# Performance work log

Hardware: AMD Instinct MI355X
Metric: run time of the kernel (lower is better)

The kernel has to match this reference:

```python
import jax, jax.numpy as jnp
import numpy as np

GROUP_NORM_EPSILON = 1e-06
NUM_GROUPS = 32


def group_norm(x, gamma, beta, num_groups, eps):
    # x: [B, H, W, C]; normalize over (H, W, C//G) within each group.
    B, H, W, C = x.shape
    xg = x.reshape(B, H, W, num_groups, C // num_groups)
    mean = jnp.mean(xg, axis=(1, 2, 4), keepdims=True)
    var = jnp.mean(jnp.square(xg - mean), axis=(1, 2, 4), keepdims=True)
    xn = (xg - mean) * jax.lax.rsqrt(var + eps)
    return xn.reshape(B, H, W, C) * gamma + beta


def setup_inputs() -> dict:
    key = jax.random.key(0)
    ks = jax.random.split(key, 6)
    B, H, W, C = 4, 64, 64, 512
    scale = 1.0 / np.sqrt(C)
    return {
        "inputs": jax.random.normal(ks[0], (B, H, W, C), dtype=jnp.float32),
        "gamma": jnp.ones((C,), dtype=jnp.float32),
        "beta": jnp.zeros((C,), dtype=jnp.float32),
        "Wq": jax.random.normal(ks[1], (C, C), dtype=jnp.float32) * scale,
        "bq": jnp.zeros((C,), dtype=jnp.float32),
        "Wk": jax.random.normal(ks[2], (C, C), dtype=jnp.float32) * scale,
        "bk": jnp.zeros((C,), dtype=jnp.float32),
        "Wv": jax.random.normal(ks[3], (C, C), dtype=jnp.float32) * scale,
        "bv": jnp.zeros((C,), dtype=jnp.float32),
        "Wo": jax.random.normal(ks[4], (C, C), dtype=jnp.float32) * scale,
        "bo": jnp.zeros((C,), dtype=jnp.float32),
    }


def reference(inputs, gamma, beta, Wq, bq, Wk, bk, Wv, bv, Wo, bo):
    B, H, W, C = inputs.shape
    N = H * W
    h = group_norm(inputs, gamma, beta, NUM_GROUPS, GROUP_NORM_EPSILON)
    hf = h.reshape(B, N, C)  # flatten spatial: [B, N, C]
    q = hf @ Wq + bq
    k = hf @ Wk + bk
    v = hf @ Wv + bv
    # full spatial self-attention: [B, N, N]
    scores = jnp.einsum("bnc,bmc->bnm", q, k) * (C ** -0.5)
    attn = jax.nn.softmax(scores, axis=-1)
    out = jnp.einsum("bnm,bmc->bnc", attn, v)
    out = out @ Wo + bo
    return out.reshape(B, H, W, C) + inputs
```

## Files before the change

### kernel.cpp

```cpp
#include <hip/hip_runtime.h>
#include <hip/hip_bf16.h>

using bf16 = __hip_bfloat16;
using u16  = unsigned short;
typedef __attribute__((ext_vector_type(8))) short s16x8;
typedef __attribute__((ext_vector_type(4))) float f32x4;

__device__ __forceinline__ float b2f(u16 u){
  union{unsigned u; float f;} c; c.u = ((unsigned)u)<<16; return c.f;
}
__device__ __forceinline__ u16 f2b(float f){
  __hip_bfloat16 h = __float2bfloat16(f);
  return *reinterpret_cast<u16*>(&h);
}

#define GLDS16(g, l_) __builtin_amdgcn_global_load_lds( \
    (const __attribute__((address_space(1))) unsigned int*)(g), \
    (__attribute__((address_space(3))) unsigned int*)(l_), 16, 0, 0)

__global__ __launch_bounds__(512) void gn_kernel(const float* __restrict__ x,
    const float* __restrict__ gamma, const float* __restrict__ beta,
    bf16* __restrict__ h)
{
  const int b = blockIdx.x >> 5, g = blockIdx.x & 31;
  const int t = threadIdx.x;
  const size_t base = (size_t)b*4096*512 + (size_t)g*16;
  float sum = 0.f, sq = 0.f;
  for (int i = 0; i < 8; i++){
    const float* p = x + base + (size_t)(i*512 + t)*512;
    #pragma unroll
    for (int j = 0; j < 4; j++){
      f32x4 v = *(const f32x4*)(p + j*4);
      #pragma unroll
      for (int e = 0; e < 4; e++){ sum += v[e]; sq += v[e]*v[e]; }
    }
  }
  __shared__ float red[16];
  for (int o = 32; o > 0; o >>= 1){ sum += __shfl_xor(sum, o); sq += __shfl_xor(sq, o); }
  const int w = t >> 6, l = t & 63;
  if (l == 0){ red[w] = sum; red[8 + w] = sq; }
  __syncthreads();
  if (t == 0){
    float a = 0.f, bb = 0.f;
    for (int i = 0; i < 8; i++){ a += red[i]; bb += red[8 + i]; }
    red[0] = a; red[8] = bb;
  }
  __syncthreads();
  const float inv_n = 1.f/65536.f;
  const float mean = red[0]*inv_n;
  const float var  = red[8]*inv_n - mean*mean;
  const float rstd = rsqrtf(var + 1e-6f);
  float ga[16], be[16];
  #pragma unroll
  for (int j = 0; j < 16; j++){
    ga[j] = gamma[g*16 + j];
    be[j] = beta [g*16 + j];
  }
  u16* hp = (u16*)h;
  for (int i = 0; i < 8; i++){
    const float* p = x + base + (size_t)(i*512 + t)*512;
    u16* q = hp + base + (size_t)(i*512 + t)*512;
    s16x8 o0, o1;
    #pragma unroll
    for (int j = 0; j < 4; j++){
      f32x4 v = *(const f32x4*)(p + j*4);
      #pragma unroll
      for (int e = 0; e < 4; e++){
        int c = j*4 + e;
        u16 r = f2b((v[e] - mean)*rstd*ga[c] + be[c]);
        if (c < 8) o0[c] = (short)r; else o1[c - 8] = (short)r;
      }
    }
    *(s16x8*)q = o0; *(s16x8*)(q + 8) = o1;
  }
}

struct W4 { const float* p[4]; };
__global__ __launch_bounds__(256) void transpose_w4(W4 srcs, bf16* __restrict__ dst)
{
  __shared__ float tile[64][65];
  const float* in = srcs.p[blockIdx.z];
  u16* out = (u16*)dst + (size_t)blockIdx.z*512*512;
  const int tr = blockIdx.y*64, tc = blockIdx.x*64;
  const int t = threadIdx.x;
  #pragma unroll
  for (int i = 0; i < 16; i++){
    int idx = i*256 + t, r = idx >> 6, c = idx & 63;
    tile[r][c] = in[(size_t)(tr + r)*512 + tc + c];
  }
  __syncthreads();
  #pragma unroll
  for (int i = 0; i < 16; i++){
    int idx = i*256 + t, r = idx >> 6, c = idx & 63;
    out[(size_t)(tc + r)*512 + tr + c] = f2b(tile[c][r]);
  }
}

template<int EPI, typename OutT>
__global__ __launch_bounds__(256) void gemm_bt(
    const u16* __restrict__ A, int lda, long sA,
    const u16* __restrict__ Bt, int ldb, long sB,
    OutT* __restrict__ Cmat, int ldc, long sC,
    int K, float scale,
    const float* __restrict__ b0, const float* __restrict__ res)
{
  __shared__ u16 As[128*64];
  __shared__ u16 Bs[128*64];
  const int t = threadIdx.x, l = t & 63, w = t >> 6;
  const int wr = w >> 1, wc = w & 1;
  int bx = blockIdx.x, by = blockIdx.y;
  {
    const int gx = gridDim.x, nb = gx * gridDim.y;
    if ((nb & 7) == 0){
      int lin = by*gx + bx;
      int s = (lin & 7)*(nb >> 3) + (lin >> 3);
      bx = s % gx; by = s / gx;
    }
  }
  const int m0 = by * 128, n0 = bx * 128;
  const u16* Au  = A  + (size_t)blockIdx.z * sA;
  const u16* Btu = Bt + (size_t)blockIdx.z * sB;

  f32x4 acc[4][4];
  #pragma unroll
  for (int m = 0; m < 4; m++)
    #pragma unroll
    for (int n = 0; n < 4; n++) acc[m][n] = (f32x4){0.f,0.f,0.f,0.f};

  const int srow = l >> 3;
  const int scol = ((l & 7) ^ srow) * 8;
  const int xorv = (l & 7) << 4;
  const int nkt = K >> 6;
  for (int kt = 0; kt < nkt; ++kt){
    const int k0 = kt << 6;
    #pragma unroll
    for (int j = 0; j < 4; j++){
      const int chunk = w*4 + j;
      const int row = chunk*8 + srow;
      GLDS16(Au  + (size_t)(m0 + row)*lda + k0 + scol, &As[chunk*512]);
      GLDS16(Btu + (size_t)(n0 + row)*ldb + k0 + scol, &Bs[chunk*512]);
    }
    __syncthreads();
    #pragma unroll
    for (int kk = 0; kk < 2; kk++){
      const int kbyte = (kk*64 + (l >> 4)*16) ^ xorv;
      s16x8 af[4], bff[4];
      #pragma unroll
      for (int m = 0; m < 4; m++)
        af[m]  = *(const s16x8*)((const char*)As + (wr*64 + m*16 + (l & 15))*128 + kbyte);
      #pragma unroll
      for (int n = 0; n < 4; n++)
        bff[n] = *(const s16x8*)((const char*)Bs + (wc*64 + n*16 + (l & 15))*128 + kbyte);
      #pragma unroll
      for (int m = 0; m < 4; m++)
        #pragma unroll
        for (int n = 0; n < 4; n++)
          acc[m][n] = __builtin_amdgcn_mfma_f32_16x16x32_bf16(af[m], bff[n], acc[m][n], 0, 0, 0);
    }
    __syncthreads();
  }
  const int lc = l & 15, lr4 = (l >> 4)*4;
  OutT* Cz = Cmat + (size_t)blockIdx.z * sC;
  #pragma unroll
  for (int n = 0; n < 4; n++){
    const int col = n0 + wc*64 + n*16 + lc;
    const float bv = (EPI & 1) ? b0[col] : 0.f;
    #pragma unroll
    for (int m = 0; m < 4; m++){
      const int rowb = m0 + wr*64 + m*16 + lr4;
      #pragma unroll
      for (int r = 0; r < 4; r++){
        float v = acc[m][n][r];
        if (EPI & 2) v *= scale;
        v += bv;
        const size_t off = (size_t)(rowb + r)*ldc + col;
        if (EPI & 4) v += res[off];
        if constexpr (__is_same(OutT, float)) Cz[off] = v;
        else ((u16*)Cz)[off] = f2b(v);
      }
    }
  }
}

template<int EPI, int OMODE>
__global__ __launch_bounds__(512, 2) void gemm256(
    const u16* __restrict__ A, int lda, long sA,
    const u16* __restrict__ Bt, int ldb, long sB,
    u16* __restrict__ C0, int ldc, long sC,
    u16* __restrict__ C1, u16* __restrict__ C2,
    int K, float scale,
    const float* __restrict__ b0, const float* __restrict__ b1,
    const float* __restrict__ b2)
{
  __shared__ u16 L[2][2][2][256*32];
  const int t = threadIdx.x, l = t & 63, w = t >> 6;
  const int wm = w >> 2, wn = w & 3;
  int bx = blockIdx.x, by = blockIdx.y;
  {
    const int gx = gridDim.x, nb = gx * gridDim.y;
    if ((nb & 7) == 0){
      int lin = by*gx + bx;
      int s = (lin & 7)*(nb >> 3) + (lin >> 3);
      bx = s % gx; by = s / gx;
    }
  }
  const int m0 = by * 256, n0 = bx * 256;
  const u16* Au  = A  + (size_t)blockIdx.z * sA;
  const u16* Btu = Bt + (size_t)blockIdx.z * sB;

  f32x4 acc[8][4];
  #pragma unroll
  for (int m = 0; m < 8; m++)
    #pragma unroll
    for (int n = 0; n < 4; n++) acc[m][n] = (f32x4){0.f,0.f,0.f,0.f};

  const int srow_s = t >> 2;
  const int sce    = (((t & 3)*16) ^ (((srow_s >> 1) & 3) << 4)) >> 1;
  const int l15 = l & 15, kb16 = (l >> 4)*16;

  int arow[8], brow[4];
  #pragma unroll
  for (int i = 0; i < 8; i++){
    const int r = wm*128 + i*16 + l15;
    arow[i] = r*64 + (kb16 ^ (((r >> 1) & 3) << 4));
  }
  #pragma unroll
  for (int i = 0; i < 4; i++){
    const int r = wn*64 + i*16 + l15;
    brow[i] = r*64 + (kb16 ^ (((r >> 1) & 3) << 4));
  }

#define STG256(HALF, XU, LD, ROW0, COLBASE) do { \
    GLDS16((XU) + (size_t)((ROW0) + srow_s)*(LD) + (COLBASE) + sce, \
           (char*)(HALF) + w*1024); \
    GLDS16((XU) + (size_t)((ROW0) + 128 + srow_s)*(LD) + (COLBASE) + sce, \
           (char*)(HALF) + 8192 + w*1024); \
  } while(0)

#define VMW4 asm volatile("s_waitcnt vmcnt(4)" ::: "memory")

#define PH256(BUF, KK, MQ, STAGE_STMT, WAIT_STMT) do { \
    s16x8 af_[4], bg_[4]; \
    _Pragma("unroll") \
    for (int mf = 0; mf < 4; mf++) \
      af_[mf] = *(const s16x8*)((const char*)&L[BUF][0][KK][0] + arow[(MQ)*4 + mf]); \
    _Pragma("unroll") \
    for (int nf = 0; nf < 4; nf++) \
      bg_[nf] = *(const s16x8*)((const char*)&L[BUF][1][KK][0] + brow[nf]); \
    STAGE_STMT; \
    WAIT_STMT; \
    __builtin_amdgcn_s_barrier(); \
    __builtin_amdgcn_s_setprio(1); \
    _Pragma("unroll") \
    for (int mf = 0; mf < 4; mf++) \
      _Pragma("unroll") \
      for (int nf = 0; nf < 4; nf++) \
        acc[(MQ)*4 + mf][nf] = __builtin_amdgcn_mfma_f32_16x16x32_bf16( \
            af_[mf], bg_[nf], acc[(MQ)*4 + mf][nf], 0, 0, 0); \
    __builtin_amdgcn_s_setprio(0); \
    __builtin_amdgcn_s_barrier(); \
  } while(0)

  const int nkt = K >> 6;
  STG256(&L[0][0][0][0], Au,  lda, m0, 0);
  STG256(&L[0][1][0][0], Btu, ldb, n0, 0);
  STG256(&L[0][0][1][0], Au,  lda, m0, 32);
  STG256(&L[0][1][1][0], Btu, ldb, n0, 32);
  STG256(&L[1][0][0][0], Au,  lda, m0, 64);
  STG256(&L[1][1][0][0], Btu, ldb, n0, 64);
  VMW4;
  __builtin_amdgcn_s_barrier();

  const int niter = nkt >> 1;
  for (int it = 0; it < niter; ++it){
    const int kt1 = 2*it + 1;
    const int kA  = (kt1 + 1 < nkt) ? kt1 + 1 : nkt - 1;
    const int kB  = (kt1 + 2 < nkt) ? kt1 + 2 : nkt - 1;
    PH256(0, 0, 0, STG256(&L[1][0][1][0], Au,  lda, m0, kt1*64 + 32), (void)0);
    PH256(0, 0, 1, STG256(&L[1][1][1][0], Btu, ldb, n0, kt1*64 + 32), (void)0);
    PH256(0, 1, 0, STG256(&L[0][0][0][0], Au,  lda, m0, kA*64),       (void)0);
    PH256(0, 1, 1, STG256(&L[0][1][0][0], Btu, ldb, n0, kA*64),       VMW4);
    PH256(1, 0, 0, STG256(&L[0][0][1][0], Au,  lda, m0, kA*64 + 32),  (void)0);
    PH256(1, 0, 1, STG256(&L[0][1][1][0], Btu, ldb, n0, kA*64 + 32),  (void)0);
    PH256(1, 1, 0, STG256(&L[1][0][0][0], Au,  lda, m0, kB*64),       (void)0);
    PH256(1, 1, 1, STG256(&L[1][1][0][0], Btu, ldb, n0, kB*64),       VMW4);
  }

  asm volatile("s_waitcnt vmcnt(0)" ::: "memory");
  __builtin_amdgcn_s_barrier();
  u16* Lb = (u16*)&L[0][0][0][0];
  const int lr4 = (l >> 4)*4;
  #pragma unroll
  for (int nf = 0; nf < 4; nf++){
    const int cloc = wn*64 + nf*16 + l15;
    const int colg = n0 + cloc;
    float bv = 0.f;
    if (EPI & 8){
      const float* bp = (colg < 512) ? b0 : (colg < 1024 ? b1 : b2);
      bv = bp[colg & 511];
    } else if (EPI & 1) bv = b0[colg];
    #pragma unroll
    for (int mf = 0; mf < 8; mf++){
      const int rl0 = wm*128 + mf*16 + lr4;
      #pragma unroll
      for (int r = 0; r < 4; r++){
        float v = acc[mf][nf][r];
        if (EPI & 2) v *= scale;
        v += bv;
        const int row = rl0 + r;
        const int byte = row*512 + ((cloc*2) ^ (((row >> 3) & 7) << 4));
        *(u16*)((char*)Lb + byte) = f2b(v);
      }
    }
  }
  __syncthreads();
  if (OMODE == 0){
    u16* Cz = C0 + (size_t)blockIdx.z * sC;
    #pragma unroll
    for (int i = 0; i < 16; i++){
      const int idx = i*512 + t;
      const int row = idx >> 5, cb = (idx & 31)*16;
      const int byte = row*512 + (cb ^ (((row >> 3) & 7) << 4));
      s16x8 v = *(const s16x8*)((const char*)Lb + byte);
      *(s16x8*)(Cz + (size_t)(m0 + row)*ldc + n0 + (cb >> 1)) = v;
    }
  } else {
    const int sec = n0 >> 9, wc0 = n0 & 511;
    if (sec < 2){
      u16* dst = (sec == 0) ? C0 : C1;
      #pragma unroll
      for (int i = 0; i < 16; i++){
        const int idx = i*512 + t;
        const int row = idx >> 5, cb = (idx & 31)*16;
        const int byte = row*512 + (cb ^ (((row >> 3) & 7) << 4));
        s16x8 v = *(const s16x8*)((const char*)Lb + byte);
        *(s16x8*)(dst + (size_t)(m0 + row)*512 + wc0 + (cb >> 1)) = v;
      }
    } else {
      const int batch = m0 >> 12, ntok = m0 & 4095;
      u16* dst = C2 + (size_t)batch*512*4096;
      #pragma unroll
      for (int i = 0; i < 16; i++){
        const int idx = i*512 + t;
        const int c_loc = idx >> 5, rseg = (idx & 31)*8;
        s16x8 v;
        #pragma unroll
        for (int j = 0; j < 8; j++){
          const int row = rseg + j;
          const int byte = row*512 + ((c_loc*2) ^ (((row >> 3) & 7) << 4));
          v[j] = *(const short*)((const char*)Lb + byte);
        }
        *(s16x8*)(dst + (size_t)(wc0 + c_loc)*4096 + ntok + rseg) = v;
      }
    }
  }
#undef STG256
#undef VMW4
#undef PH256
}

__global__ __launch_bounds__(512) void pv_fused(
    const u16* __restrict__ S, const u16* __restrict__ vT,
    bf16* __restrict__ ao, int batched, int batch0)
{
  __shared__ u16 Bs[256*64];
  __shared__ u16 Ps[64*64];
  __shared__ float lsArr[64];
  const int t = threadIdx.x, l = t & 63, w = t >> 6;
  int batch, mt, half;
  if (batched){
    const int lin = blockIdx.x, x = lin & 7, s = lin >> 3;
    batch = x >> 1; mt = (s >> 1)*2 + (x & 1); half = s & 1;
  } else { batch = batch0; mt = blockIdx.x >> 1; half = blockIdx.x & 1; }
  const int m0 = mt*64, c0 = half*256;
  const u16* Sb  = S  + (size_t)batch*4096*4096;
  const u16* vTb = vT + (size_t)batch*512*4096 + (size_t)c0*4096;
  u16* aob = (u16*)ao + (size_t)batch*4096*512;

  f32x4 acc[4][2];
  #pragma unroll
  for (int m = 0; m < 4; m++)
    #pragma unroll
    for (int n = 0; n < 2; n++) acc[m][n] = (f32x4){0.f,0.f,0.f,0.f};

  const int srow = l >> 3, lane8 = l & 7;
  const int scol = (lane8 ^ srow) * 8;
  const int xorv = lane8 << 4;
  const int r_loc = w*8 + srow;
  const int smaddr = r_loc*128 + ((lane8*16) ^ (srow << 4));
  float lsumrow = 0.f;

  const u16* Srow = Sb + (size_t)(m0 + r_loc)*4096 + lane8*8;

  #pragma unroll
  for (int j = 0; j < 4; j++){
    const int chunk = w*4 + j;
    const int row = chunk*8 + srow;
    GLDS16(vTb + (size_t)row*4096 + scol, &Bs[chunk*512]);
  }
  s16x8 S_cur = *(const s16x8*)Srow;

  for (int kt = 0; kt < 64; ++kt){
    const int ktn = (kt < 63) ? kt + 1 : 63;
    s16x8 S_next = *(const s16x8*)(Srow + ktn*64);

    s16x8 pb;
    #pragma unroll
    for (int j = 0; j < 8; j++){
      const float pvv = exp2f(fminf(b2f((u16)S_cur[j]), 100.f));
      lsumrow += pvv;
      pb[j] = (short)f2b(pvv);
    }

    *(s16x8*)((char*)Ps + smaddr) = pb;

    asm volatile("s_waitcnt lgkmcnt(0)" ::: "memory");
    __builtin_amdgcn_sched_barrier(0);
    asm volatile("s_waitcnt vmcnt(1)" ::: "memory");
    __builtin_amdgcn_sched_barrier(0);
    __builtin_amdgcn_s_barrier();

    #pragma unroll
    for (int kk = 0; kk < 2; kk++){
      const int kbyte = (kk*64 + (l >> 4)*16) ^ xorv;
      s16x8 pa[4], bf2[2];
      #pragma unroll
      for (int m = 0; m < 4; m++)
        pa[m] = *(const s16x8*)((const char*)Ps + (m*16 + (l & 15))*128 + kbyte);
      #pragma unroll
      for (int n = 0; n < 2; n++)
        bf2[n] = *(const s16x8*)((const char*)Bs + (w*32 + n*16 + (l & 15))*128 + kbyte);
      #pragma unroll
      for (int m = 0; m < 4; m++)
        #pragma unroll
        for (int n = 0; n < 2; n++)
          acc[m][n] = __builtin_amdgcn_mfma_f32_16x16x32_bf16(pa[m], bf2[n], acc[m][n], 0, 0, 0);
    }

    __builtin_amdgcn_sched_barrier(0);
    __builtin_amdgcn_s_barrier();
    __builtin_amdgcn_sched_barrier(0);

    #pragma unroll
    for (int j = 0; j < 4; j++){
      const int chunk = w*4 + j;
      const int row = chunk*8 + srow;
      GLDS16(vTb + (size_t)row*4096 + ktn*64 + scol, &Bs[chunk*512]);
    }
    S_cur = S_next;
  }

  lsumrow += __shfl_xor(lsumrow, 1);
  lsumrow += __shfl_xor(lsumrow, 2);
  lsumrow += __shfl_xor(lsumrow, 4);
  if (lane8 == 0) lsArr[r_loc] = lsumrow;
  __syncthreads();
  #pragma unroll
  for (int m = 0; m < 4; m++){
    const f32x4 lq = *(const f32x4*)&lsArr[m*16 + (l >> 4)*4];
    #pragma unroll
    for (int r = 0; r < 4; r++){
      const float inv = 1.f / lq[r];
      const int row = m0 + m*16 + (l >> 4)*4 + r;
      #pragma unroll
      for (int n = 0; n < 2; n++){
        const int col = c0 + w*32 + n*16 + (l & 15);
        aob[(size_t)row*512 + col] = f2b(acc[m][n][r] * inv);
      }
    }
  }
}

extern "C" void kernel_launch(void* const* d_in, const int* in_sizes, int n_in,
                              void* d_out, int out_size, void* d_ws, size_t ws_size,
                              hipStream_t stream)
{
  (void)in_sizes; (void)n_in; (void)out_size;
  const float* x     = (const float*)d_in[0];
  const float* gamma = (const float*)d_in[1];
  const float* beta  = (const float*)d_in[2];
  const float* Wq = (const float*)d_in[3]; const float* bq = (const float*)d_in[4];
  const float* Wk = (const float*)d_in[5]; const float* bk = (const float*)d_in[6];
  const float* Wv = (const float*)d_in[7]; const float* bv = (const float*)d_in[8];
  const float* Wo = (const float*)d_in[9]; const float* bo = (const float*)d_in[10];
  float* out = (float*)d_out;

  const int B = 4, N = 4096, C = 512;
  const long NC = (long)N*C;
  const float scl2 = 0.04419417382415922f * 1.4426950408889634f;

  char* p0 = (char*)d_ws;
  auto align = [](size_t b){ return (b + 255) & ~(size_t)255; };
  const size_t sz_h  = align((size_t)B*NC*2);
  const size_t sz_w  = align((size_t)4*C*C*2);
  const size_t sz_q  = align((size_t)B*NC*2);
  const size_t sz_S  = align((size_t)B*N*N*2);
  const size_t need_full = sz_h + sz_w + 4*sz_q + sz_S;

  bf16* h    = (bf16*)p0;
  bf16* wAll = (bf16*)(p0 + sz_h);
  char* pv   = p0 + sz_h + sz_w;
  bf16* woT  = wAll + (size_t)3*C*C;

  gn_kernel<<<dim3(B*32), dim3(512), 0, stream>>>(x, gamma, beta, h);
  W4 ws4; ws4.p[0] = Wq; ws4.p[1] = Wk; ws4.p[2] = Wv; ws4.p[3] = Wo;
  transpose_w4<<<dim3(8, 8, 4), 256, 0, stream>>>(ws4, wAll);

  if (ws_size >= need_full){
    u16* q  = (u16*)pv;
    u16* k  = (u16*)(pv + sz_q);
    u16* vT = (u16*)(pv + 2*sz_q);
    u16* ao = (u16*)(pv + 3*sz_q);
    u16* S  = (u16*)(pv + 4*sz_q);

    gemm256<8, 1><<<dim3(6, 64, 1), 512, 0, stream>>>(
        (const u16*)h, C, 0, (const u16*)wAll, C, 0,
        q, 0, 0, k, vT, C, 1.f, bq, bk, bv);
    gemm256<2, 0><<<dim3(16, 16, B), 512, 0, stream>>>(
        q, C, NC, k, C, NC, S, N, (long)N*N, nullptr, nullptr,
        C, scl2, nullptr, nullptr, nullptr);
    pv_fused<<<dim3(512), 512, 0, stream>>>(
        S, vT, (bf16*)ao, 1, 0);
    gemm_bt<5, float><<<dim3(4, 128, 1), 256, 0, stream>>>(
        ao, C, 0, (const u16*)woT, C, 0, out, C, 0,
        C, 1.f, bo, x);
  } else {
    u16* q  = (u16*)pv;
    u16* k  = (u16*)(pv + sz_q/4 + 256);
    u16* vT = (u16*)(pv + 2*(sz_q/4 + 256));
    u16* ao = (u16*)(pv + 3*(sz_q/4 + 256));
    u16* S  = (u16*)(pv + 4*(sz_q/4 + 256));
    for (int b = 0; b < B; b++){
      const u16* hb = (const u16*)h + (size_t)b*NC;
      gemm256<8, 1><<<dim3(6, 16, 1), 512, 0, stream>>>(
          hb, C, 0, (const u16*)wAll, C, 0,
          q, 0, 0, k, vT, C, 1.f, bq, bk, bv);
      gemm256<2, 0><<<dim3(16, 16, 1), 512, 0, stream>>>(
          q, C, 0, k, C, 0, S, N, 0, nullptr, nullptr,
          C, scl2, nullptr, nullptr, nullptr);
      pv_fused<<<dim3(128), 512, 0, stream>>>(
          S, vT, (bf16*)ao, 0, 0);
      gemm_bt<5, float><<<dim3(4, 32, 1), 256, 0, stream>>>(
          ao, C, 0, (const u16*)woT, C, 0, out + (size_t)b*NC, C, 0,
          C, 1.f, bo, x + (size_t)b*NC);
    }
  }
}
```

Measured before the change: 401.6 us.

## Fuse exp2 and row-sum into QK^T epilogue, double-buffer PV via LDS loads

The QK^T GEMM epilogue now applies exp2 to the scaled scores, writes P in bf16, and atomically accumulates per-row sums into a workspace buffer that gn_kernel zeroes. The PV kernel no longer does exp per element. It streams P and V^T into double-buffered LDS with direct global-to-LDS loads, raises priority around the MFMAs, and reads the row sums at the end. This removes exp work and the register-path S loads from the PV loop and overlaps loads with compute. The cost is global atomics and doubled LDS, which may cut occupancy. The sum is now taken over unrounded values while P is stored rounded to bf16.

```diff
diff --git a/kernel.cpp b/kernel.cpp
--- a/kernel.cpp
+++ b/kernel.cpp
@@ -20,10 +20,11 @@
 
 __global__ __launch_bounds__(512) void gn_kernel(const float* __restrict__ x,
     const float* __restrict__ gamma, const float* __restrict__ beta,
-    bf16* __restrict__ h)
+    bf16* __restrict__ h, float* __restrict__ rsum)
 {
   const int b = blockIdx.x >> 5, g = blockIdx.x & 31;
   const int t = threadIdx.x;
+  if (t < 128) rsum[blockIdx.x*128 + t] = 0.f;
   const size_t base = (size_t)b*4096*512 + (size_t)g*16;
   float sum = 0.f, sq = 0.f;
   for (int i = 0; i < 8; i++){
@@ -182,7 +183,7 @@
   }
 }
 
-template<int EPI, int OMODE>
+template<int EPI, int OMODE, int EXP2>
 __global__ __launch_bounds__(512, 2) void gemm256(
     const u16* __restrict__ A, int lda, long sA,
     const u16* __restrict__ Bt, int ldb, long sB,
@@ -190,7 +191,7 @@
     u16* __restrict__ C1, u16* __restrict__ C2,
     int K, float scale,
     const float* __restrict__ b0, const float* __restrict__ b1,
-    const float* __restrict__ b2)
+    const float* __restrict__ b2, float* __restrict__ rsum)
 {
   __shared__ u16 L[2][2][2][256*32];
   const int t = threadIdx.x, l = t & 63, w = t >> 6;
@@ -290,26 +291,49 @@
   __builtin_amdgcn_s_barrier();
   u16* Lb = (u16*)&L[0][0][0][0];
   const int lr4 = (l >> 4)*4;
-  #pragma unroll
-  for (int nf = 0; nf < 4; nf++){
-    const int cloc = wn*64 + nf*16 + l15;
-    const int colg = n0 + cloc;
-    float bv = 0.f;
-    if (EPI & 8){
-      const float* bp = (colg < 512) ? b0 : (colg < 1024 ? b1 : b2);
-      bv = bp[colg & 511];
-    } else if (EPI & 1) bv = b0[colg];
+  if (EXP2){
     #pragma unroll
     for (int mf = 0; mf < 8; mf++){
-      const int rl0 = wm*128 + mf*16 + lr4;
       #pragma unroll
       for (int r = 0; r < 4; r++){
-        float v = acc[mf][nf][r];
-        if (EPI & 2) v *= scale;
-        v += bv;
-        const int row = rl0 + r;
-        const int byte = row*512 + ((cloc*2) ^ (((row >> 3) & 7) << 4));
-        *(u16*)((char*)Lb + byte) = f2b(v);
+        const int row = wm*128 + mf*16 + lr4 + r;
+        float s = 0.f;
+        #pragma unroll
+        for (int nf = 0; nf < 4; nf++){
+          const int cloc = wn*64 + nf*16 + l15;
+          float v = exp2f(fminf(acc[mf][nf][r]*scale, 100.f));
+          s += v;
+          const int byte = row*512 + ((cloc*2) ^ (((row >> 3) & 7) << 4));
+          *(u16*)((char*)Lb + byte) = f2b(v);
+        }
+        s += __shfl_xor(s, 1); s += __shfl_xor(s, 2);
+        s += __shfl_xor(s, 4); s += __shfl_xor(s, 8);
+        if (l15 == 0)
+          atomicAdd(rsum + (size_t)blockIdx.z*4096 + m0 + row, s);
+      }
+    }
+  } else {
+    #pragma unroll
+    for (int nf = 0; nf < 4; nf++){
+      const int cloc = wn*64 + nf*16 + l15;
+      const int colg = n0 + cloc;
+      float bv = 0.f;
+      if (EPI & 8){
+        const float* bp = (colg < 512) ? b0 : (colg < 1024 ? b1 : b2);
+        bv = bp[colg & 511];
+      } else if (EPI & 1) bv = b0[colg];
+      #pragma unroll
+      for (int mf = 0; mf < 8; mf++){
+        const int rl0 = wm*128 + mf*16 + lr4;
+        #pragma unroll
+        for (int r = 0; r < 4; r++){
+          float v = acc[mf][nf][r];
+          if (EPI & 2) v *= scale;
+          v += bv;
+          const int row = rl0 + r;
+          const int byte = row*512 + ((cloc*2) ^ (((row >> 3) & 7) << 4));
+          *(u16*)((char*)Lb + byte) = f2b(v);
+        }
       }
     }
   }
@@ -359,12 +383,13 @@
 #undef PH256
 }
 
-__global__ __launch_bounds__(512) void pv_fused(
-    const u16* __restrict__ S, const u16* __restrict__ vT,
-    bf16* __restrict__ ao, int batched, int batch0)
+__global__ __launch_bounds__(512, 2) void pv_fused(
+    const u16* __restrict__ P, const u16* __restrict__ vT,
+    const float* __restrict__ rsum, bf16* __restrict__ ao,
+    int batched, int batch0)
 {
-  __shared__ u16 Bs[256*64];
-  __shared__ u16 Ps[64*64];
+  __shared__ u16 Bs[2][256*64];
+  __shared__ u16 Ps[2][64*64];
   __shared__ float lsArr[64];
   const int t = threadIdx.x, l = t & 63, w = t >> 6;
   int batch, mt, half;
@@ -373,7 +398,7 @@
     batch = x >> 1; mt = (s >> 1)*2 + (x & 1); half = s & 1;
   } else { batch = batch0; mt = blockIdx.x >> 1; half = blockIdx.x & 1; }
   const int m0 = mt*64, c0 = half*256;
-  const u16* Sb  = S  + (size_t)batch*4096*4096;
+  const u16* Pb  = P  + (size_t)batch*4096*4096;
   const u16* vTb = vT + (size_t)batch*512*4096 + (size_t)c0*4096;
   u16* aob = (u16*)ao + (size_t)batch*4096*512;
 
@@ -386,74 +411,56 @@
   const int srow = l >> 3, lane8 = l & 7;
   const int scol = (lane8 ^ srow) * 8;
   const int xorv = lane8 << 4;
-  const int r_loc = w*8 + srow;
-  const int smaddr = r_loc*128 + ((lane8*16) ^ (srow << 4));
-  float lsumrow = 0.f;
-
-  const u16* Srow = Sb + (size_t)(m0 + r_loc)*4096 + lane8*8;
-
-  #pragma unroll
-  for (int j = 0; j < 4; j++){
-    const int chunk = w*4 + j;
-    const int row = chunk*8 + srow;
-    GLDS16(vTb + (size_t)row*4096 + scol, &Bs[chunk*512]);
-  }
-  s16x8 S_cur = *(const s16x8*)Srow;
+
+#define PVSTAGE(BUF, KT) do { \
+    const int k0_ = (KT)*64; \
+    _Pragma("unroll") \
+    for (int j = 0; j < 4; j++){ \
+      const int chunk = w*4 + j; \
+      GLDS16(vTb + (size_t)(chunk*8 + srow)*4096 + k0_ + scol, &Bs[BUF][chunk*512]); \
+    } \
+    GLDS16(Pb + (size_t)(m0 + w*8 + srow)*4096 + k0_ + scol, &Ps[BUF][w*512]); \
+  } while(0)
+
+  PVSTAGE(0, 0);
+  PVSTAGE(1, 1);
 
   for (int kt = 0; kt < 64; ++kt){
-    const int ktn = (kt < 63) ? kt + 1 : 63;
-    s16x8 S_next = *(const s16x8*)(Srow + ktn*64);
-
-    s16x8 pb;
-    #pragma unroll
-    for (int j = 0; j < 8; j++){
-      const float pvv = exp2f(fminf(b2f((u16)S_cur[j]), 100.f));
-      lsumrow += pvv;
-      pb[j] = (short)f2b(pvv);
-    }
-
-    *(s16x8*)((char*)Ps + smaddr) = pb;
-
-    asm volatile("s_waitcnt lgkmcnt(0)" ::: "memory");
-    __builtin_amdgcn_sched_barrier(0);
-    asm volatile("s_waitcnt vmcnt(1)" ::: "memory");
+    const int buf = kt & 1;
+    asm volatile("s_waitcnt vmcnt(5)" ::: "memory");
     __builtin_amdgcn_sched_barrier(0);
     __builtin_amdgcn_s_barrier();
 
+    __builtin_amdgcn_s_setprio(1);
     #pragma unroll
     for (int kk = 0; kk < 2; kk++){
       const int kbyte = (kk*64 + (l >> 4)*16) ^ xorv;
       s16x8 pa[4], bf2[2];
       #pragma unroll
       for (int m = 0; m < 4; m++)
-        pa[m] = *(const s16x8*)((const char*)Ps + (m*16 + (l & 15))*128 + kbyte);
+        pa[m] = *(const s16x8*)((const char*)&Ps[buf][0] + (m*16 + (l & 15))*128 + kbyte);
       #pragma unroll
       for (int n = 0; n < 2; n++)
-        bf2[n] = *(const s16x8*)((const char*)Bs + (w*32 + n*16 + (l & 15))*128 + kbyte);
+        bf2[n] = *(const s16x8*)((const char*)&Bs[buf][0] + (w*32 + n*16 + (l & 15))*128 + kbyte);
       #pragma unroll
       for (int m = 0; m < 4; m++)
         #pragma unroll
         for (int n = 0; n < 2; n++)
           acc[m][n] = __builtin_amdgcn_mfma_f32_16x16x32_bf16(pa[m], bf2[n], acc[m][n], 0, 0, 0);
     }
+    __builtin_amdgcn_s_setprio(0);
 
     __builtin_amdgcn_sched_barrier(0);
     __builtin_amdgcn_s_barrier();
     __builtin_amdgcn_sched_barrier(0);
 
-    #pragma unroll
-    for (int j = 0; j < 4; j++){
-      const int chunk = w*4 + j;
-      const int row = chunk*8 + srow;
-      GLDS16(vTb + (size_t)row*4096 + ktn*64 + scol, &Bs[chunk*512]);
-    }
-    S_cur = S_next;
-  }
-
-  lsumrow += __shfl_xor(lsumrow, 1);
-  lsumrow += __shfl_xor(lsumrow, 2);
-  lsumrow += __shfl_xor(lsumrow, 4);
-  if (lane8 == 0) lsArr[r_loc] = lsumrow;
+    const int ktn = (kt + 2 < 64) ? kt + 2 : 63;
+    PVSTAGE(buf, ktn);
+  }
+#undef PVSTAGE
+
+  __syncthreads();
+  if (t < 64) lsArr[t] = rsum[(size_t)batch*4096 + m0 + t];
   __syncthreads();
   #pragma unroll
   for (int m = 0; m < 4; m++){
@@ -493,16 +500,18 @@
   auto align = [](size_t b){ return (b + 255) & ~(size_t)255; };
   const size_t sz_h  = align((size_t)B*NC*2);
   const size_t sz_w  = align((size_t)4*C*C*2);
+  const size_t sz_rs = align((size_t)B*N*4);
   const size_t sz_q  = align((size_t)B*NC*2);
   const size_t sz_S  = align((size_t)B*N*N*2);
-  const size_t need_full = sz_h + sz_w + 4*sz_q + sz_S;
-
-  bf16* h    = (bf16*)p0;
-  bf16* wAll = (bf16*)(p0 + sz_h);
-  char* pv   = p0 + sz_h + sz_w;
-  bf16* woT  = wAll + (size_t)3*C*C;
-
-  gn_kernel<<<dim3(B*32), dim3(512), 0, stream>>>(x, gamma, beta, h);
+  const size_t need_full = sz_h + sz_w + sz_rs + 4*sz_q + sz_S;
+
+  bf16*  h    = (bf16*)p0;
+  bf16*  wAll = (bf16*)(p0 + sz_h);
+  float* rsum = (float*)(p0 + sz_h + sz_w);
+  char*  pv   = p0 + sz_h + sz_w + sz_rs;
+  bf16*  woT  = wAll + (size_t)3*C*C;
+
+  gn_kernel<<<dim3(B*32), dim3(512), 0, stream>>>(x, gamma, beta, h, rsum);
   W4 ws4; ws4.p[0] = Wq; ws4.p[1] = Wk; ws4.p[2] = Wv; ws4.p[3] = Wo;
   transpose_w4<<<dim3(8, 8, 4), 256, 0, stream>>>(ws4, wAll);
 
@@ -511,35 +520,37 @@
     u16* k  = (u16*)(pv + sz_q);
     u16* vT = (u16*)(pv + 2*sz_q);
     u16* ao = (u16*)(pv + 3*sz_q);
-    u16* S  = (u16*)(pv + 4*sz_q);
-
-    gemm256<8, 1><<<dim3(6, 64, 1), 512, 0, stream>>>(
+    u16* P  = (u16*)(pv + 4*sz_q);
+
+    gemm256<8, 1, 0><<<dim3(6, 64, 1), 512, 0, stream>>>(
         (const u16*)h, C, 0, (const u16*)wAll, C, 0,
-        q, 0, 0, k, vT, C, 1.f, bq, bk, bv);
-    gemm256<2, 0><<<dim3(16, 16, B), 512, 0, stream>>>(
-        q, C, NC, k, C, NC, S, N, (long)N*N, nullptr, nullptr,
-        C, scl2, nullptr, nullptr, nullptr);
+        q, 0, 0, k, vT, C, 1.f, bq, bk, bv, nullptr);
+    gemm256<2, 0, 1><<<dim3(16, 16, B), 512, 0, stream>>>(
+        q, C, NC, k, C, NC, P, N, (long)N*N, nullptr, nullptr,
+        C, scl2, nullptr, nullptr, nullptr, rsum);
     pv_fused<<<dim3(512), 512, 0, stream>>>(
-        S, vT, (bf16*)ao, 1, 0);
+        P, vT, rsum, (bf16*)ao, 1, 0);
     gemm_bt<5, float><<<dim3(4, 128, 1), 256, 0, stream>>>(
         ao, C, 0, (const u16*)woT, C, 0, out, C, 0,
         C, 1.f, bo, x);
   } else {
+    const size_t sz_q1 = align((size_t)NC*2);
     u16* q  = (u16*)pv;
-    u16* k  = (u16*)(pv + sz_q/4 + 256);
-    u16* vT = (u16*)(pv + 2*(sz_q/4 + 256));
-    u16* ao = (u16*)(pv + 3*(sz_q/4 + 256));
-    u16* S  = (u16*)(pv + 4*(sz_q/4 + 256));
+    u16* k  = (u16*)(pv + sz_q1);
+    u16* vT = (u16*)(pv + 2*sz_q1);
+    u16* ao = (u16*)(pv + 3*sz_q1);
+    u16* P  = (u16*)(pv + 4*sz_q1);
     for (int b = 0; b < B; b++){
       const u16* hb = (const u16*)h + (size_t)b*NC;
-      gemm256<8, 1><<<dim3(6, 16, 1), 512, 0, stream>>>(
+      float* rsb = rsum + (size_t)b*N;
+      gemm256<8, 1, 0><<<dim3(6, 16, 1), 512, 0, stream>>>(
           hb, C, 0, (const u16*)wAll, C, 0,
-          q, 0, 0, k, vT, C, 1.f, bq, bk, bv);
-      gemm256<2, 0><<<dim3(16, 16, 1), 512, 0, stream>>>(
-          q, C, 0, k, C, 0, S, N, 0, nullptr, nullptr,
-          C, scl2, nullptr, nullptr, nullptr);
+          q, 0, 0, k, vT, C, 1.f, bq, bk, bv, nullptr);
+      gemm256<2, 0, 1><<<dim3(16, 16, 1), 512, 0, stream>>>(
+          q, C, 0, k, C, 0, P, N, 0, nullptr, nullptr,
+          C, scl2, nullptr, nullptr, nullptr, rsb);
       pv_fused<<<dim3(128), 512, 0, stream>>>(
-          S, vT, (bf16*)ao, 0, 0);
+          P, vT, rsb, (bf16*)ao, 0, 0);
       gemm_bt<5, float><<<dim3(4, 32, 1), 256, 0, stream>>>(
           ao, C, 0, (const u16*)woT, C, 0, out + (size_t)b*NC, C, 0,
           C, 1.f, bo, x + (size_t)b*NC);
```

Result: slower. 457.2 us (+13.9%).
